# Optimization experiments

Hardware: AMD Instinct MI355X
Metric: run time of the kernel (lower is better)

## Reference

```python
import jax, jax.numpy as jnp
import numpy as np

OUT_CHANNELS = 16
PH = PW = 7          # output_size
SR = 2               # sampling_ratio


def setup_inputs() -> dict:
    key = jax.random.key(0)
    k1, k2, k3, k4 = jax.random.split(key, 4)
    B, C, H, W = 4, OUT_CHANNELS * PH * PW, 80, 80
    feat = jax.random.normal(k1, (B, C, H, W), dtype=jnp.float32)
    N = 512
    bidx = jax.random.randint(k2, (N,), 0, B).astype(jnp.float32)
    tl = jax.random.uniform(k3, (N, 2), minval=0.0, maxval=0.7)   # x1, y1 (normalized)
    sz = jax.random.uniform(k4, (N, 2), minval=0.05, maxval=0.3)  # box size
    rois = jnp.concatenate([bidx[:, None], tl, tl + sz], axis=1)  # [N,5]
    return {"input": feat, "rois": rois}


def _psroi_one(feat_ps, roi):
    # feat_ps: [B, Co, PH, PW, H, W]  (position-sensitive channel layout)
    B, Co, _, _, H, W = feat_ps.shape
    f = feat_ps[roi[0].astype(jnp.int32)]              # [Co, PH, PW, H, W]
    x1 = roi[1] * W; y1 = roi[2] * H
    x2 = roi[3] * W; y2 = roi[4] * H                   # adaptive spatial_scale = (H, W)
    roi_h = jnp.maximum(y2 - y1, 0.1)
    roi_w = jnp.maximum(x2 - x1, 0.1)
    bin_h = roi_h / PH
    bin_w = roi_w / PW
    # sample coordinates per bin: [PH,SR] and [PW,SR]
    ys = y1 + jnp.arange(PH, dtype=f.dtype)[:, None] * bin_h + (jnp.arange(SR, dtype=f.dtype)[None, :] + 0.5) * bin_h / SR
    xs = x1 + jnp.arange(PW, dtype=f.dtype)[:, None] * bin_w + (jnp.arange(SR, dtype=f.dtype)[None, :] + 0.5) * bin_w / SR
    ym = (ys >= -1.0) & (ys <= H)
    xm = (xs >= -1.0) & (xs <= W)
    yc = jnp.clip(ys, 0.0, H - 1)
    xc = jnp.clip(xs, 0.0, W - 1)
    y0 = jnp.floor(yc).astype(jnp.int32)
    x0 = jnp.floor(xc).astype(jnp.int32)
    y1i = jnp.minimum(y0 + 1, H - 1)
    x1i = jnp.minimum(x0 + 1, W - 1)
    ly = yc - y0.astype(f.dtype); hy = 1.0 - ly        # [PH,SR]
    lx = xc - x0.astype(f.dtype); hx = 1.0 - lx        # [PW,SR]
    I = jnp.arange(PH)[:, None, None, None]            # bin row index
    J = jnp.arange(PW)[None, None, :, None]            # bin col index

    def g(Y, X):
        # gather f[c, i, j, Y[i,sy], X[j,sx]] -> [Co, PH, SR, PW, SR]
        return f[:, I, J, Y[:, :, None, None], X[None, None, :, :]]

    v = (g(y0, x0)  * (hy[:, :, None, None] * hx[None, None])
       + g(y0, x1i) * (hy[:, :, None, None] * lx[None, None])
       + g(y1i, x0) * (ly[:, :, None, None] * hx[None, None])
       + g(y1i, x1i) * (ly[:, :, None, None] * lx[None, None]))
    v = v * (ym[:, :, None, None] & xm[None, None]).astype(v.dtype)
    return v.mean(axis=(2, 4))                          # [Co, PH, PW]


def reference(input, rois):
    B, C, H, W = input.shape
    feat_ps = input.reshape(B, OUT_CHANNELS, PH, PW, H, W)
    rois = rois.reshape(-1, 5)
    out = jax.vmap(lambda r: _psroi_one(feat_ps, r))(rois)  # [N, Co, PH, PW]
    return out
```

## Files before the change

### kernel.cpp

```cpp
#include <hip/hip_runtime.h>

#define NB   4
#define CO   16
#define PH   7
#define PW   7
#define SR   2
#define HH   80
#define WW   80
#define NROI 512
#define CIJ  (CO*PH*PW)
#define PLANE (HH*WW)
#define NF4  (PLANE/4)

typedef float f4v __attribute__((ext_vector_type(4), aligned(16)));

typedef __attribute__((address_space(1))) const void gvoid_t;
typedef __attribute__((address_space(3))) void svoid_t;

#define WS_ORDER_OFF 64
#define WS_GEOM_OFF  2048

__global__ __launch_bounds__(512) void psroi_prep_kernel(
    const float* __restrict__ rois, int* __restrict__ base,
    unsigned short* __restrict__ order, f4v* __restrict__ geom)
{
    __shared__ int cnt[NB];
    __shared__ int cbase[NB + 1];
    int n = threadIdx.x;
    if (n < NB) cnt[n] = 0;
    __syncthreads();
    int b = (int)rois[n * 5 + 0];
    int rank = atomicAdd(&cnt[b], 1);
    __syncthreads();
    if (n == 0) {
        cbase[0] = 0;
        for (int k = 0; k < NB; ++k) cbase[k + 1] = cbase[k] + cnt[k];
        for (int k = 0; k <= NB; ++k) base[k] = cbase[k];
    }
    __syncthreads();
    int pos = cbase[b] + rank;
    order[pos] = (unsigned short)n;

    float x1 = rois[n * 5 + 1] * (float)WW;
    float y1 = rois[n * 5 + 2] * (float)HH;
    float x2 = rois[n * 5 + 3] * (float)WW;
    float y2 = rois[n * 5 + 4] * (float)HH;
    f4v g;
    g.x = x1;
    g.y = y1;
    g.z = fmaxf(x2 - x1, 0.1f) * (1.0f / PW);
    g.w = fmaxf(y2 - y1, 0.1f) * (1.0f / PH);
    geom[pos] = g;
}

__global__ __launch_bounds__(256) void psroi_main_kernel(
    const float* __restrict__ feat,
    const int* __restrict__ base,
    const unsigned short* __restrict__ order,
    const f4v* __restrict__ geom,
    float* __restrict__ out)
{
    __shared__ __align__(16) float sp[PLANE];

    int u   = blockIdx.x;
    int cij = u >> 2;
    int b   = u & 3;
    int rem = cij % (PH * PW);
    int i = rem / PW;
    int j = rem % PW;
    int n = threadIdx.x;

    const f4v* src = (const f4v*)(feat + ((size_t)b * CIJ + (size_t)cij) * PLANE);
    int wbase = n & ~63;
    #pragma unroll
    for (int it = 0; it < 6; ++it) {
        const f4v* g = src + it * 256 + n;
        float* l = sp + (size_t)(it * 256 + wbase) * 4;
        __builtin_amdgcn_global_load_lds((gvoid_t*)g, (svoid_t*)l, 16, 0, 0);
    }
    if (n < 64) {
        const f4v* g = src + 1536 + n;
        float* l = sp + (size_t)1536 * 4;
        __builtin_amdgcn_global_load_lds((gvoid_t*)g, (svoid_t*)l, 16, 0, 0);
    }

    int lo = base[b];
    int hi = base[b + 1];

    __syncthreads();

    int sy = n & 1;
    float sy_off = ((float)sy + 0.5f) * (1.0f / SR);

    for (int t = lo + (n >> 1); t < hi; t += 128) {
        int m = (int)order[t];
        f4v g = geom[t];
        float x1 = g.x, y1 = g.y, bin_w = g.z, bin_h = g.w;

        float ys = y1 + ((float)i + sy_off) * bin_h;
        bool ymask = (ys >= -1.0f) && (ys <= (float)HH);
        float yc = fminf(fmaxf(ys, 0.0f), (float)(HH - 1));
        int   y0 = (int)floorf(yc);
        int   y1i = min(y0 + 1, HH - 1);
        float ly = yc - (float)y0, hy = 1.0f - ly;

        float partial = 0.0f;
        #pragma unroll
        for (int sx = 0; sx < SR; ++sx) {
            float xs = x1 + ((float)j + ((float)sx + 0.5f) * (1.0f / SR)) * bin_w;
            bool xmask = (xs >= -1.0f) && (xs <= (float)WW);
            float xc = fminf(fmaxf(xs, 0.0f), (float)(WW - 1));
            int   x0 = (int)floorf(xc);
            int   x0c = min(x0, WW - 2);
            bool  sh = (x0 != x0c);
            float lx = xc - (float)x0, hx = 1.0f - lx;

            float t0 = sp[y0  * WW + x0c], t1 = sp[y0  * WW + x0c + 1];
            float b0 = sp[y1i * WW + x0c], b1 = sp[y1i * WW + x0c + 1];

            float v00 = sh ? t1 : t0;
            float v10 = sh ? b1 : b0;
            float v = (v00 * hx + t1 * lx) * hy + (v10 * hx + b1 * lx) * ly;
            if (ymask && xmask) partial += v;
        }

        float other = __shfl_xor(partial, 1);
        if (sy == 0)
            out[(size_t)m * CIJ + cij] = (partial + other) * 0.25f;
    }
}

extern "C" void kernel_launch(void* const* d_in, const int* in_sizes, int n_in,
                              void* d_out, int out_size, void* d_ws, size_t ws_size,
                              hipStream_t stream)
{
    const float* feat = (const float*)d_in[0];
    const float* rois = (const float*)d_in[1];
    float* out = (float*)d_out;

    char* ws = (char*)d_ws;
    int* base = (int*)ws;
    unsigned short* order = (unsigned short*)(ws + WS_ORDER_OFF);
    f4v* geom = (f4v*)(ws + WS_GEOM_OFF);

    psroi_prep_kernel<<<1, NROI, 0, stream>>>(rois, base, order, geom);
    psroi_main_kernel<<<CIJ * NB, 256, 0, stream>>>(feat, base, order, geom, out);
}
```

Baseline: 111.8 us.

## Fuse ROI bucketing into main kernel, dropping separate prep launch

Removes the single-block prep kernel that sorted ROIs by batch index and precomputed geometry. Each main-kernel block now builds its own per-batch ROI list in shared memory with ballot/popcount compaction while its feature plane streams into LDS, then recomputes geometry from raw rois. This trades a second launch and its serialization for redundant per-block scanning of 512 ROIs and a changed, non-sorted ROI order within each batch.

```diff
diff --git a/kernel.cpp b/kernel.cpp
--- a/kernel.cpp
+++ b/kernel.cpp
@@ -13,54 +13,19 @@
 #define NF4  (PLANE/4)
 
 typedef float f4v __attribute__((ext_vector_type(4), aligned(16)));
+typedef float f4u __attribute__((ext_vector_type(4), aligned(4)));
 
 typedef __attribute__((address_space(1))) const void gvoid_t;
 typedef __attribute__((address_space(3))) void svoid_t;
 
-#define WS_ORDER_OFF 64
-#define WS_GEOM_OFF  2048
-
-__global__ __launch_bounds__(512) void psroi_prep_kernel(
-    const float* __restrict__ rois, int* __restrict__ base,
-    unsigned short* __restrict__ order, f4v* __restrict__ geom)
-{
-    __shared__ int cnt[NB];
-    __shared__ int cbase[NB + 1];
-    int n = threadIdx.x;
-    if (n < NB) cnt[n] = 0;
-    __syncthreads();
-    int b = (int)rois[n * 5 + 0];
-    int rank = atomicAdd(&cnt[b], 1);
-    __syncthreads();
-    if (n == 0) {
-        cbase[0] = 0;
-        for (int k = 0; k < NB; ++k) cbase[k + 1] = cbase[k] + cnt[k];
-        for (int k = 0; k <= NB; ++k) base[k] = cbase[k];
-    }
-    __syncthreads();
-    int pos = cbase[b] + rank;
-    order[pos] = (unsigned short)n;
-
-    float x1 = rois[n * 5 + 1] * (float)WW;
-    float y1 = rois[n * 5 + 2] * (float)HH;
-    float x2 = rois[n * 5 + 3] * (float)WW;
-    float y2 = rois[n * 5 + 4] * (float)HH;
-    f4v g;
-    g.x = x1;
-    g.y = y1;
-    g.z = fmaxf(x2 - x1, 0.1f) * (1.0f / PW);
-    g.w = fmaxf(y2 - y1, 0.1f) * (1.0f / PH);
-    geom[pos] = g;
-}
-
 __global__ __launch_bounds__(256) void psroi_main_kernel(
     const float* __restrict__ feat,
-    const int* __restrict__ base,
-    const unsigned short* __restrict__ order,
-    const f4v* __restrict__ geom,
+    const float* __restrict__ rois,
     float* __restrict__ out)
 {
     __shared__ __align__(16) float sp[PLANE];
+    __shared__ unsigned short list[NROI];
+    __shared__ int cnt;
 
     int u   = blockIdx.x;
     int cij = u >> 2;
@@ -69,6 +34,7 @@
     int i = rem / PW;
     int j = rem % PW;
     int n = threadIdx.x;
+    int lane = n & 63;
 
     const f4v* src = (const f4v*)(feat + ((size_t)b * CIJ + (size_t)cij) * PLANE);
     int wbase = n & ~63;
@@ -84,18 +50,34 @@
         __builtin_amdgcn_global_load_lds((gvoid_t*)g, (svoid_t*)l, 16, 0, 0);
     }
 
-    int lo = base[b];
-    int hi = base[b + 1];
+    if (n == 0) cnt = 0;
+    __syncthreads();
+    #pragma unroll
+    for (int pass = 0; pass < 2; ++pass) {
+        int m = n + pass * 256;
+        bool hit = ((int)rois[m * 5] == b);
+        unsigned long long mask = __ballot(hit);
+        int before = __popcll(mask & ((1ULL << lane) - 1ULL));
+        int total  = __popcll(mask);
+        int wb = 0;
+        if (lane == 0 && total) wb = atomicAdd(&cnt, total);
+        wb = __shfl(wb, 0);
+        if (hit) list[wb + before] = (unsigned short)m;
+    }
 
     __syncthreads();
+    int count = cnt;
 
     int sy = n & 1;
     float sy_off = ((float)sy + 0.5f) * (1.0f / SR);
 
-    for (int t = lo + (n >> 1); t < hi; t += 128) {
-        int m = (int)order[t];
-        f4v g = geom[t];
-        float x1 = g.x, y1 = g.y, bin_w = g.z, bin_h = g.w;
+    for (int t = (n >> 1); t < count; t += 128) {
+        int m = (int)list[t];
+        f4u g = *(const f4u*)(rois + m * 5 + 1);
+        float x1 = g.x * (float)WW;
+        float y1 = g.y * (float)HH;
+        float bin_w = fmaxf(g.z * (float)WW - x1, 0.1f) * (1.0f / PW);
+        float bin_h = fmaxf(g.w * (float)HH - y1, 0.1f) * (1.0f / PH);
 
         float ys = y1 + ((float)i + sy_off) * bin_h;
         bool ymask = (ys >= -1.0f) && (ys <= (float)HH);
@@ -138,11 +120,5 @@
     const float* rois = (const float*)d_in[1];
     float* out = (float*)d_out;
 
-    char* ws = (char*)d_ws;
-    int* base = (int*)ws;
-    unsigned short* order = (unsigned short*)(ws + WS_ORDER_OFF);
-    f4v* geom = (f4v*)(ws + WS_GEOM_OFF);
-
-    psroi_prep_kernel<<<1, NROI, 0, stream>>>(rois, base, order, geom);
-    psroi_main_kernel<<<CIJ * NB, 256, 0, stream>>>(feat, base, order, geom, out);
+    psroi_main_kernel<<<CIJ * NB, 256, 0, stream>>>(feat, rois, out);
 }
```

New measurement: 113.1 us. No clear change (+1.1%).

## Write ROI outputs to transposed scratch, then transpose via shared-memory tile kernel

Applied to the files above, without the earlier changes.

The main kernel now writes results contiguously per channel-bin into a workspace buffer indexed by sorted ROI position, instead of scattering each value to out[m*CIJ+cij] with a large stride. A new third kernel transposes this buffer through a shared-memory tile and uses the order array to place rows in the final output layout. This aims to replace strided, uncoalesced stores with coalesced ones, at the cost of an extra launch and an extra round trip through global memory for the output.

```diff
diff --git a/kernel.cpp b/kernel.cpp
--- a/kernel.cpp
+++ b/kernel.cpp
@@ -19,6 +19,7 @@
 
 #define WS_ORDER_OFF 64
 #define WS_GEOM_OFF  2048
+#define WS_OUTT_OFF  16384
 
 __global__ __launch_bounds__(512) void psroi_prep_kernel(
     const float* __restrict__ rois, int* __restrict__ base,
@@ -56,9 +57,8 @@
 __global__ __launch_bounds__(256) void psroi_main_kernel(
     const float* __restrict__ feat,
     const int* __restrict__ base,
-    const unsigned short* __restrict__ order,
     const f4v* __restrict__ geom,
-    float* __restrict__ out)
+    float* __restrict__ out_t)
 {
     __shared__ __align__(16) float sp[PLANE];
 
@@ -86,15 +86,15 @@
 
     int lo = base[b];
     int hi = base[b + 1];
+    int count = hi - lo;
 
     __syncthreads();
 
     int sy = n & 1;
     float sy_off = ((float)sy + 0.5f) * (1.0f / SR);
 
-    for (int t = lo + (n >> 1); t < hi; t += 128) {
-        int m = (int)order[t];
-        f4v g = geom[t];
+    for (int t = (n >> 1); t < count; t += 128) {
+        f4v g = geom[lo + t];
         float x1 = g.x, y1 = g.y, bin_w = g.z, bin_h = g.w;
 
         float ys = y1 + ((float)i + sy_off) * bin_h;
@@ -126,7 +126,39 @@
 
         float other = __shfl_xor(partial, 1);
         if (sy == 0)
-            out[(size_t)m * CIJ + cij] = (partial + other) * 0.25f;
+            out_t[(size_t)cij * NROI + lo + t] = (partial + other) * 0.25f;
+    }
+}
+
+__global__ __launch_bounds__(256) void psroi_tr_kernel(
+    const float* __restrict__ out_t,
+    const unsigned short* __restrict__ order,
+    float* __restrict__ out)
+{
+    __shared__ float tile[64][17];
+
+    int gx = blockIdx.x % 49;
+    int gp = blockIdx.x / 49;
+    int cij0 = gx * 16;
+    int p0 = gp * 64;
+    int tid = threadIdx.x;
+
+    int c  = tid & 63;
+    int r4 = tid >> 6;
+    #pragma unroll
+    for (int rr = 0; rr < 4; ++rr) {
+        int r = r4 * 4 + rr;
+        tile[c][r] = out_t[(size_t)(cij0 + r) * NROI + p0 + c];
+    }
+    __syncthreads();
+
+    int cj = tid & 15;
+    int pq = tid >> 4;
+    #pragma unroll
+    for (int ch = 0; ch < 4; ++ch) {
+        int pp = ch * 16 + pq;
+        int m = (int)order[p0 + pp];
+        out[(size_t)m * CIJ + cij0 + cj] = tile[pp][cj];
     }
 }
 
@@ -142,7 +174,9 @@
     int* base = (int*)ws;
     unsigned short* order = (unsigned short*)(ws + WS_ORDER_OFF);
     f4v* geom = (f4v*)(ws + WS_GEOM_OFF);
+    float* out_t = (float*)(ws + WS_OUTT_OFF);
 
     psroi_prep_kernel<<<1, NROI, 0, stream>>>(rois, base, order, geom);
-    psroi_main_kernel<<<CIJ * NB, 256, 0, stream>>>(feat, base, order, geom, out);
+    psroi_main_kernel<<<CIJ * NB, 256, 0, stream>>>(feat, base, geom, out_t);
+    psroi_tr_kernel<<<49 * 8, 256, 0, stream>>>(out_t, order, out);
 }
```

Result: slower. 114.9 us (+2.7%).
